# Kernel optimization log

Measured on AMD Instinct MI355X. Metric: run time of the kernel, lower is better.

## Reference

```python
import jax, jax.numpy as jnp
import numpy as np

F, H, K, T, IT, S = 128, 128, 768, 4, 2, 57  # feat, hidden, max_child, edge types, iters, num_sem


def setup_inputs() -> dict:
    key = jax.random.key(0)
    ks = jax.random.split(key, 12)

    def w(k, shape):
        fan = shape[0] if len(shape) == 2 else shape[1]
        return jax.random.normal(k, shape, jnp.float32) * fan ** -0.5

    return {
        "parent_feature": jax.random.normal(ks[0], (1, F), jnp.float32),
        "W_parent": w(ks[1], (F, H * K)), "b_parent": jnp.zeros((H * K,), jnp.float32),
        "W_exists": w(ks[2], (H, 1)), "b_exists": jnp.zeros((1,), jnp.float32),
        "W_edge_lat": w(ks[3], (2 * H, H)), "b_edge_lat": jnp.zeros((H,), jnp.float32),
        "W_edge_ex": w(ks[4], (T, H)), "b_edge_ex": jnp.zeros((T,), jnp.float32),
        "W_ne": w(ks[5], (IT, 2 * H, H)), "b_ne": jnp.zeros((IT, H), jnp.float32),
        "W_child": w(ks[6], (H * (IT + 1), H)), "b_child": jnp.zeros((H,), jnp.float32),
        "W_sem": w(ks[7], (H, S)), "b_sem": jnp.zeros((S,), jnp.float32),
        "W_child2": w(ks[8], (H, F)), "b_child2": jnp.zeros((F,), jnp.float32),
    }


def reference(parent_feature, W_parent, b_parent, W_exists, b_exists,
              W_edge_lat, b_edge_lat, W_edge_ex, b_edge_ex,
              W_ne, b_ne, W_child, b_child, W_sem, b_sem, W_child2, b_child2):
    # parent -> K child latents
    x = jax.nn.relu(parent_feature @ W_parent + b_parent)  # [1, K*H]
    cf = x.reshape(1, K, H)                                 # child feats
    exists_logits = cf @ W_exists + b_exists                # [1, K, 1]

    # pairwise edge latents [1, K, K, 2H] -> [1, K, K, H]
    pair0 = jnp.concatenate([
        jnp.broadcast_to(cf[:, :, None, :], (1, K, K, H)),
        jnp.broadcast_to(cf[:, None, :, :], (1, K, K, H))], axis=3)
    elat = jax.nn.relu(pair0 @ W_edge_lat + b_edge_lat)
    edge_logits = jnp.einsum('bijh,th->bijt', elat, W_edge_ex) + b_edge_ex  # [1,K,K,T]

    # fixed edge set: existing edges between existing nodes (dense mask form)
    exists = exists_logits[0, :, 0] > 0                     # [K]
    emask = jnp.any(edge_logits[0] > 0, axis=-1) & exists[:, None] & exists[None, :]
    any_edge = jnp.any(emask)

    feats = [cf]
    for i in range(IT):
        c = cf[0]                                           # [K, H]
        pair = jnp.concatenate([
            jnp.broadcast_to(c[:, None, :], (K, K, H)),
            jnp.broadcast_to(c[None, :, :], (K, K, H))], axis=2)
        msg = jax.nn.relu(pair @ W_ne[i] + b_ne[i])         # [K, K, H], >= 0
        msg = jnp.where(emask[:, :, None], msg, 0.0)
        # scatter_max with zeros-initialized out == max over masked neighbors (msg >= 0)
        new_cf = msg.max(axis=1)[None]                      # [1, K, H]
        cf = jnp.where(any_edge, new_cf, cf)                # no edges -> feats unchanged
        feats.append(cf)

    h = jnp.concatenate(feats, axis=2).reshape(K, H * (IT + 1))
    h = jax.nn.relu(h @ W_child + b_child)                  # [K, H]
    sem_logits = (h @ W_sem + b_sem).reshape(1, K, S)
    child_out = jax.nn.relu(h @ W_child2 + b_child2).reshape(1, K, F)
    return child_out, sem_logits, exists_logits, edge_logits
```

## Files before the change

### kernel.cpp

```cpp
#include <hip/hip_runtime.h>
#include <hip/hip_bf16.h>


#define NK 768
#define NH 128
#define NCF 98304

typedef float v2f __attribute__((ext_vector_type(2)));

__global__ __launch_bounds__(512) void k_pd(const float* __restrict__ pf,
    const float* __restrict__ Wp, const float* __restrict__ bp,
    const float* __restrict__ Wexi, const float* __restrict__ bexi,
    const float* __restrict__ Wel, const float* __restrict__ bel,
    const float* __restrict__ Wne, const float* __restrict__ Wee,
    float* __restrict__ cf0g, float* __restrict__ exO,
    float* __restrict__ A_T, float* __restrict__ BT,
    float* __restrict__ A0, float* __restrict__ B0,
    float* __restrict__ WeeT, unsigned int* __restrict__ flag)
{
    __shared__ float s_pf[128];
    __shared__ float s_cf0[2][128];
    __shared__ __align__(16) char s_scr[16384];
    int t = threadIdx.x;
    int b = blockIdx.x;
    int k0 = 2 * b;
    if (t < 128) s_pf[t] = pf[t];
    if (b == 0 && t == 0) *flag = 0u;
    if (b == 0) WeeT[(t & 127) * 4 + (t >> 7)] = Wee[t];
    __syncthreads();
    {
        float4* s_part = (float4*)s_scr;
        int c = t & 63, g = t >> 6;
        const float4* W4 = (const float4*)Wp;
        size_t base = (size_t)b * 64 + c;
        float4 acc = make_float4(0.f, 0.f, 0.f, 0.f);
        #pragma unroll
        for (int q = 0; q < 16; ++q) {
            int f = g * 16 + q;
            float4 w = W4[(size_t)f * 24576 + base];
            float p = s_pf[f];
            acc.x = fmaf(p, w.x, acc.x);
            acc.y = fmaf(p, w.y, acc.y);
            acc.z = fmaf(p, w.z, acc.z);
            acc.w = fmaf(p, w.w, acc.w);
        }
        s_part[g * 64 + c] = acc;
        __syncthreads();
        if (t < 64) {
            float4 r = s_part[t];
            #pragma unroll
            for (int g2 = 1; g2 < 8; ++g2) {
                float4 p = s_part[g2 * 64 + t];
                r.x += p.x; r.y += p.y; r.z += p.z; r.w += p.w;
            }
            float4 bi = ((const float4*)bp)[b * 64 + t];
            r.x = fmaxf(r.x + bi.x, 0.f);
            r.y = fmaxf(r.y + bi.y, 0.f);
            r.z = fmaxf(r.z + bi.z, 0.f);
            r.w = fmaxf(r.w + bi.w, 0.f);
            int row = t >> 5, h4 = t & 31;
            *(float4*)&s_cf0[row][h4 * 4] = r;
            ((float4*)cf0g)[(size_t)b * 64 + t] = r;
            float4 w = ((const float4*)Wexi)[h4];
            float dot = r.x * w.x + r.y * w.y + r.z * w.z + r.w * w.w;
            dot += __shfl_xor(dot, 16);
            dot += __shfl_xor(dot, 8);
            dot += __shfl_xor(dot, 4);
            dot += __shfl_xor(dot, 2);
            dot += __shfl_xor(dot, 1);
            if (h4 == 0) exO[k0 + row] = dot + bexi[0];
        }
    }
    __syncthreads();
    {
        float4* s_p2 = (float4*)s_scr;
        int mat = t >> 7, q = (t >> 5) & 3, c = t & 31;
        const float* W = (mat == 0) ? Wel : (mat == 1) ? (Wel + 16384)
                       : (mat == 2) ? Wne : (Wne + 16384);
        float4 a0 = make_float4(0.f, 0.f, 0.f, 0.f);
        float4 a1 = make_float4(0.f, 0.f, 0.f, 0.f);
        #pragma unroll 8
        for (int x = q * 32; x < q * 32 + 32; ++x) {
            float4 w = *(const float4*)&W[x * 128 + c * 4];
            float c0 = s_cf0[0][x], c1 = s_cf0[1][x];
            a0.x = fmaf(c0, w.x, a0.x); a0.y = fmaf(c0, w.y, a0.y);
            a0.z = fmaf(c0, w.z, a0.z); a0.w = fmaf(c0, w.w, a0.w);
            a1.x = fmaf(c1, w.x, a1.x); a1.y = fmaf(c1, w.y, a1.y);
            a1.z = fmaf(c1, w.z, a1.z); a1.w = fmaf(c1, w.w, a1.w);
        }
        s_p2[((mat * 4 + q) * 2 + 0) * 32 + c] = a0;
        s_p2[((mat * 4 + q) * 2 + 1) * 32 + c] = a1;
        __syncthreads();
        if (t < 256) {
            int m2 = t >> 6, row = (t >> 5) & 1, c2 = t & 31;
            float4 r = s_p2[((m2 * 4 + 0) * 2 + row) * 32 + c2];
            #pragma unroll
            for (int q2 = 1; q2 < 4; ++q2) {
                float4 p = s_p2[((m2 * 4 + q2) * 2 + row) * 32 + c2];
                r.x += p.x; r.y += p.y; r.z += p.z; r.w += p.w;
            }
            if (m2 == 0) {
                float4 bl = *(const float4*)&bel[c2 * 4];
                A_T[(size_t)(c2 * 4 + 0) * NK + k0 + row] = r.x + bl.x;
                A_T[(size_t)(c2 * 4 + 1) * NK + k0 + row] = r.y + bl.y;
                A_T[(size_t)(c2 * 4 + 2) * NK + k0 + row] = r.z + bl.z;
                A_T[(size_t)(c2 * 4 + 3) * NK + k0 + row] = r.w + bl.w;
            } else if (m2 == 1) {
                BT[(c2 * 4 + 0) * NK + k0 + row] = r.x;
                BT[(c2 * 4 + 1) * NK + k0 + row] = r.y;
                BT[(c2 * 4 + 2) * NK + k0 + row] = r.z;
                BT[(c2 * 4 + 3) * NK + k0 + row] = r.w;
            } else if (m2 == 2) {
                ((float4*)A0)[(size_t)(k0 + row) * 32 + c2] = r;
            } else {
                ((float4*)B0)[(size_t)(k0 + row) * 32 + c2] = r;
            }
        }
    }
}

__global__ __launch_bounds__(256) void k_edge(const float* __restrict__ A_T,
    const float* __restrict__ BT, const float* __restrict__ WeeT,
    const float* __restrict__ bex, const float* __restrict__ exO,
    float* __restrict__ edge_out, unsigned char* __restrict__ mask,
    unsigned int* __restrict__ flag)
{
    __shared__ float s_B[2][16][256];
    __shared__ float s_exi[4];
    __shared__ unsigned int s_any;
    int t = threadIdx.x;
    int i0 = blockIdx.x * 4;
    int j = blockIdx.y * 256 + t;
    float exj = exO[j];
    if (t < 4) s_exi[t] = exO[i0 + t];
    if (t == 0) s_any = 0u;
    const float4* BT4 = (const float4*)BT;
    int row = t >> 6, col = t & 63;
    {
        #pragma unroll
        for (int k = 0; k < 4; ++k)
            *(float4*)&s_B[0][row + k * 4][col * 4] =
                BT4[(size_t)(row + k * 4) * 192 + blockIdx.y * 64 + col];
    }
    __syncthreads();
    v2f l01[4] = {}, l23[4] = {};
    for (int c = 0; c < 8; ++c) {
        float4 r0, r1, r2, r3;
        if (c < 7) {
            size_t base = (size_t)((c + 1) * 16 + row) * 192 + blockIdx.y * 64 + col;
            r0 = BT4[base];
            r1 = BT4[base + 4 * 192];
            r2 = BT4[base + 8 * 192];
            r3 = BT4[base + 12 * 192];
        }
        int buf = c & 1;
        #pragma unroll
        for (int hh = 0; hh < 16; ++hh) {
            int h = c * 16 + hh;
            float4 av = *(const float4*)&A_T[(size_t)h * NK + i0];
            float4 wv = *(const float4*)&WeeT[h * 4];
            float bv = s_B[buf][hh][t];
            v2f e01 = __builtin_elementwise_max((v2f){av.x + bv, av.y + bv}, (v2f){0.f, 0.f});
            v2f e23 = __builtin_elementwise_max((v2f){av.z + bv, av.w + bv}, (v2f){0.f, 0.f});
            l01[0] += e01 * wv.x; l01[1] += e01 * wv.y;
            l01[2] += e01 * wv.z; l01[3] += e01 * wv.w;
            l23[0] += e23 * wv.x; l23[1] += e23 * wv.y;
            l23[2] += e23 * wv.z; l23[3] += e23 * wv.w;
        }
        if (c < 7) {
            int nb = (c + 1) & 1;
            *(float4*)&s_B[nb][row + 0][col * 4] = r0;
            *(float4*)&s_B[nb][row + 4][col * 4] = r1;
            *(float4*)&s_B[nb][row + 8][col * 4] = r2;
            *(float4*)&s_B[nb][row + 12][col * 4] = r3;
        }
        __syncthreads();
    }
    float b0 = bex[0], b1 = bex[1], b2 = bex[2], b3 = bex[3];
    bool ej = exj > 0.f;
    float4 v0 = make_float4(l01[0].x + b0, l01[1].x + b1, l01[2].x + b2, l01[3].x + b3);
    float4 v1 = make_float4(l01[0].y + b0, l01[1].y + b1, l01[2].y + b2, l01[3].y + b3);
    float4 v2 = make_float4(l23[0].x + b0, l23[1].x + b1, l23[2].x + b2, l23[3].x + b3);
    float4 v3 = make_float4(l23[0].y + b0, l23[1].y + b1, l23[2].y + b2, l23[3].y + b3);
    ((float4*)edge_out)[(size_t)(i0 + 0) * NK + j] = v0;
    ((float4*)edge_out)[(size_t)(i0 + 1) * NK + j] = v1;
    ((float4*)edge_out)[(size_t)(i0 + 2) * NK + j] = v2;
    ((float4*)edge_out)[(size_t)(i0 + 3) * NK + j] = v3;
    bool m0 = ((v0.x > 0.f) | (v0.y > 0.f) | (v0.z > 0.f) | (v0.w > 0.f)) && ej && (s_exi[0] > 0.f);
    bool m1 = ((v1.x > 0.f) | (v1.y > 0.f) | (v1.z > 0.f) | (v1.w > 0.f)) && ej && (s_exi[1] > 0.f);
    bool m2 = ((v2.x > 0.f) | (v2.y > 0.f) | (v2.z > 0.f) | (v2.w > 0.f)) && ej && (s_exi[2] > 0.f);
    bool m3 = ((v3.x > 0.f) | (v3.y > 0.f) | (v3.z > 0.f) | (v3.w > 0.f)) && ej && (s_exi[3] > 0.f);
    mask[(i0 + 0) * NK + j] = m0 ? (unsigned char)1 : (unsigned char)0;
    mask[(i0 + 1) * NK + j] = m1 ? (unsigned char)1 : (unsigned char)0;
    mask[(i0 + 2) * NK + j] = m2 ? (unsigned char)1 : (unsigned char)0;
    mask[(i0 + 3) * NK + j] = m3 ? (unsigned char)1 : (unsigned char)0;
    unsigned long long bal = __ballot((m0 | m1 | m2 | m3) ? 1 : 0);
    if ((t & 63) == 0 && bal) s_any = 1u;
    __syncthreads();
    if (t == 0 && s_any) *flag = 1u;
}

__global__ __launch_bounds__(256) void k_mm(const float* __restrict__ Bm,
    const unsigned char* __restrict__ mask, float* __restrict__ Mp)
{
    __shared__ float s_B[32][128];
    __shared__ float s_madd[96][8];
    int t = threadIdx.x;
    int i0 = blockIdx.x * 8;
    int j0 = blockIdx.y * 96;
    for (int idx = t; idx < 768; idx += 256) {
        int jj = idx >> 3, i = idx & 7;
        s_madd[jj][i] = mask[(i0 + i) * NK + j0 + jj] ? 0.f : -1e30f;
    }
    int p = t & 63, g = t >> 6;
    v2f M0 = {-1e30f, -1e30f}, M1 = {-1e30f, -1e30f};
    const float4* B4 = (const float4*)Bm;
    for (int c = 0; c < 3; ++c) {
        __syncthreads();
        #pragma unroll
        for (int k = 0; k < 4; ++k) {
            int idx = t + k * 256;
            ((float4*)s_B)[idx] = B4[(size_t)(j0 + c * 32) * 32 + idx];
        }
        __syncthreads();
        #pragma unroll 8
        for (int jj = 0; jj < 32; ++jj) {
            v2f b = *(const v2f*)&s_B[jj][2 * p];
            float m0 = s_madd[c * 32 + jj][2 * g];
            float m1 = s_madd[c * 32 + jj][2 * g + 1];
            M0 = __builtin_elementwise_max(M0, b + (v2f){m0, m0});
            M1 = __builtin_elementwise_max(M1, b + (v2f){m1, m1});
        }
    }
    float* Mb = Mp + (size_t)blockIdx.y * NCF;
    *(v2f*)&Mb[(i0 + 2 * g) * 128 + 2 * p] = M0;
    *(v2f*)&Mb[(i0 + 2 * g + 1) * 128 + 2 * p] = M1;
}

__global__ __launch_bounds__(512) void k_cmb1(const float* __restrict__ Mp,
    const float* __restrict__ A0, const float* __restrict__ bne,
    const float* __restrict__ cf0, const unsigned int* __restrict__ flag,
    float* __restrict__ cf1, const float* __restrict__ Wne1,
    float* __restrict__ A1, float* __restrict__ B1)
{
    __shared__ float s_cf[2][128];
    int t = threadIdx.x;
    int k0 = blockIdx.x * 2;
    unsigned int fl = *flag;
    if (t < 256) {
        int kk = t >> 7, hh = t & 127;
        int g = (k0 + kk) * 128 + hh;
        float M = Mp[g];
        #pragma unroll
        for (int q = 1; q < 8; ++q) M = fmaxf(M, Mp[q * NCF + g]);
        float v = fl ? fmaxf(A0[g] + bne[hh] + M, 0.f) : cf0[g];
        s_cf[kk][hh] = v;
        cf1[g] = v;
    }
    __syncthreads();
    int h = t & 127, kk = (t >> 7) & 1, half = t >> 8;
    const float* W = Wne1 + half * 16384;
    const float* c = &s_cf[kk][0];
    float acc = 0.f;
    #pragma unroll 8
    for (int r = 0; r < 128; ++r)
        acc = fmaf(c[r], W[r * 128 + h], acc);
    float* D = half ? B1 : A1;
    D[(k0 + kk) * 128 + h] = acc;
}

__global__ __launch_bounds__(512) void k_final(const float* __restrict__ cf0,
    const float* __restrict__ cf1, const float* __restrict__ Mp,
    const float* __restrict__ A1, const float* __restrict__ bne1,
    const unsigned int* __restrict__ flag,
    const float* __restrict__ Wc, const float* __restrict__ bc,
    const float* __restrict__ Wsem, const float* __restrict__ bsem,
    const float* __restrict__ W2, const float* __restrict__ b2,
    float* __restrict__ out)
{
    __shared__ float s_f[2][384];
    __shared__ float s_h[2][128];
    __shared__ float s_hp[2][128];
    int t = threadIdx.x;
    int k0 = blockIdx.x * 2;
    unsigned int fl = *flag;
    for (int idx = t; idx < 768; idx += 512) {
        int kk = idx >= 384 ? 1 : 0;
        int c = idx - kk * 384;
        int row = k0 + kk;
        float v;
        if (c < 128) v = cf0[row * 128 + c];
        else if (c < 256) v = cf1[row * 128 + (c - 128)];
        else {
            int hh = c - 256, g = row * 128 + hh;
            float M = Mp[g];
            #pragma unroll
            for (int q = 1; q < 8; ++q) M = fmaxf(M, Mp[q * NCF + g]);
            v = fl ? fmaxf(A1[g] + bne1[hh] + M, 0.f) : cf1[g];
        }
        s_f[kk][c] = v;
    }
    __syncthreads();
    int h = t & 127, rh = (t >> 7) & 1, kg = t >> 8;
    float acc = 0.f;
    {
        const float* f = &s_f[kg][rh * 192];
        const float* Wcp = Wc + rh * 192 * 128;
        #pragma unroll 8
        for (int r = 0; r < 192; ++r)
            acc = fmaf(f[r], Wcp[r * 128 + h], acc);
    }
    if (rh) s_hp[kg][h] = acc;
    __syncthreads();
    if (!rh) s_h[kg][h] = fmaxf(acc + s_hp[kg][h] + bc[h], 0.f);
    __syncthreads();
    float a2 = 0.f;
    {
        const float* hr = &s_h[kg][rh * 64];
        const float* W2p = W2 + rh * 64 * 128;
        #pragma unroll 8
        for (int r = 0; r < 64; ++r)
            a2 = fmaf(hr[r], W2p[r * 128 + h], a2);
    }
    if (rh) s_hp[kg][h] = a2;
    __syncthreads();
    if (!rh) out[(size_t)(k0 + kg) * 128 + h] = fmaxf(a2 + s_hp[kg][h] + b2[h], 0.f);
    if (t < 114) {
        int kk = t / 57, sidx = t - kk * 57;
        float ss = bsem[sidx];
        const float* hr = &s_h[kk][0];
        #pragma unroll 8
        for (int r = 0; r < 128; ++r)
            ss = fmaf(hr[r], Wsem[r * 57 + sidx], ss);
        out[98304 + (size_t)(k0 + kk) * 57 + sidx] = ss;
    }
}

extern "C" void kernel_launch(void* const* d_in, const int* in_sizes, int n_in,
                              void* d_out, int out_size, void* d_ws, size_t ws_size,
                              hipStream_t stream) {
    const float* pf   = (const float*)d_in[0];
    const float* Wp   = (const float*)d_in[1];
    const float* bp   = (const float*)d_in[2];
    const float* Wexi = (const float*)d_in[3];
    const float* bexi = (const float*)d_in[4];
    const float* Wel  = (const float*)d_in[5];
    const float* bel  = (const float*)d_in[6];
    const float* Wee  = (const float*)d_in[7];
    const float* bee  = (const float*)d_in[8];
    const float* Wne  = (const float*)d_in[9];
    const float* bne  = (const float*)d_in[10];
    const float* Wc   = (const float*)d_in[11];
    const float* bc   = (const float*)d_in[12];
    const float* Wsem = (const float*)d_in[13];
    const float* bsem = (const float*)d_in[14];
    const float* W2   = (const float*)d_in[15];
    const float* b2   = (const float*)d_in[16];
    float* out = (float*)d_out;
    float* ws  = (float*)d_ws;
    const int N = NCF;
    float* cf0 = ws;
    float* cf1 = ws + N;
    float* A_T = ws + 2 * N;
    float* BT  = ws + 3 * N;
    float* A0  = ws + 4 * N;
    float* B0  = ws + 5 * N;
    float* A1  = ws + 6 * N;
    float* B1  = ws + 7 * N;
    float* Mp  = ws + 8 * N;
    float* WeeT = ws + 16 * N;
    unsigned char* mask = (unsigned char*)(ws + 16 * N + 512);
    unsigned int* flag  = (unsigned int*)(mask + 589824);

    float* out_ex   = out + 142080;
    float* out_edge = out + 142848;

    k_pd<<<384, 512, 0, stream>>>(pf, Wp, bp, Wexi, bexi, Wel, bel, Wne, Wee,
                                  cf0, out_ex, A_T, BT, A0, B0, WeeT, flag);
    k_edge<<<dim3(192, 3), 256, 0, stream>>>(A_T, BT, WeeT, bee, out_ex,
                                             out_edge, mask, flag);
    k_mm<<<dim3(96, 8), 256, 0, stream>>>(B0, mask, Mp);
    k_cmb1<<<384, 512, 0, stream>>>(Mp, A0, bne, cf0, flag, cf1, Wne + 32768, A1, B1);
    k_mm<<<dim3(96, 8), 256, 0, stream>>>(B1, mask, Mp);
    k_final<<<384, 512, 0, stream>>>(cf0, cf1, Mp, A1, bne + 128, flag,
                                     Wc, bc, Wsem, bsem, W2, b2, out);
}
```

Measured before the change: 81.83 us.

## Fuse masked max-reduction into combine and final kernels, drop partial buffer

Removes the standalone masked-max kernel and its 8-way partial-max buffer. Each 2-row block of the combine and final kernels now computes the full masked max over all 768 neighbours itself: four thread groups each stream 192 rows of B from global memory, and the partial maxima are reduced in shared memory. This cuts two launches and the partial-buffer write/read round trip. In exchange, each block rereads the whole 384 KB B matrix from L2, where the old kernel reused B tiles staged in shared memory across 8 rows.

```diff
diff --git a/kernel.cpp b/kernel.cpp
--- a/kernel.cpp
+++ b/kernel.cpp
@@ -200,65 +200,48 @@
     if (t == 0 && s_any) *flag = 1u;
 }
 
-__global__ __launch_bounds__(256) void k_mm(const float* __restrict__ Bm,
-    const unsigned char* __restrict__ mask, float* __restrict__ Mp)
+__global__ __launch_bounds__(512) void k_msgA(const float* __restrict__ B0,
+    const unsigned char* __restrict__ mask, const float* __restrict__ A0,
+    const float* __restrict__ bne, const float* __restrict__ cf0,
+    const unsigned int* __restrict__ flag, float* __restrict__ cf1,
+    const float* __restrict__ Wne1, float* __restrict__ A1, float* __restrict__ B1)
 {
-    __shared__ float s_B[32][128];
-    __shared__ float s_madd[96][8];
-    int t = threadIdx.x;
-    int i0 = blockIdx.x * 8;
-    int j0 = blockIdx.y * 96;
-    for (int idx = t; idx < 768; idx += 256) {
-        int jj = idx >> 3, i = idx & 7;
-        s_madd[jj][i] = mask[(i0 + i) * NK + j0 + jj] ? 0.f : -1e30f;
-    }
-    int p = t & 63, g = t >> 6;
-    v2f M0 = {-1e30f, -1e30f}, M1 = {-1e30f, -1e30f};
-    const float4* B4 = (const float4*)Bm;
-    for (int c = 0; c < 3; ++c) {
-        __syncthreads();
-        #pragma unroll
-        for (int k = 0; k < 4; ++k) {
-            int idx = t + k * 256;
-            ((float4*)s_B)[idx] = B4[(size_t)(j0 + c * 32) * 32 + idx];
-        }
-        __syncthreads();
-        #pragma unroll 8
-        for (int jj = 0; jj < 32; ++jj) {
-            v2f b = *(const v2f*)&s_B[jj][2 * p];
-            float m0 = s_madd[c * 32 + jj][2 * g];
-            float m1 = s_madd[c * 32 + jj][2 * g + 1];
-            M0 = __builtin_elementwise_max(M0, b + (v2f){m0, m0});
-            M1 = __builtin_elementwise_max(M1, b + (v2f){m1, m1});
-        }
-    }
-    float* Mb = Mp + (size_t)blockIdx.y * NCF;
-    *(v2f*)&Mb[(i0 + 2 * g) * 128 + 2 * p] = M0;
-    *(v2f*)&Mb[(i0 + 2 * g + 1) * 128 + 2 * p] = M1;
-}
-
-__global__ __launch_bounds__(512) void k_cmb1(const float* __restrict__ Mp,
-    const float* __restrict__ A0, const float* __restrict__ bne,
-    const float* __restrict__ cf0, const unsigned int* __restrict__ flag,
-    float* __restrict__ cf1, const float* __restrict__ Wne1,
-    float* __restrict__ A1, float* __restrict__ B1)
-{
+    __shared__ float s_madd[2][768];
+    __shared__ float s_red[2][512];
     __shared__ float s_cf[2][128];
     int t = threadIdx.x;
     int k0 = blockIdx.x * 2;
+    for (int idx = t; idx < 1536; idx += 512) {
+        int r = idx >= 768 ? 1 : 0, jj = idx - r * 768;
+        s_madd[r][jj] = mask[(k0 + r) * NK + jj] ? 0.f : -1e30f;
+    }
+    __syncthreads();
+    int h = t & 127, q = t >> 7;
+    float M0 = -1e30f, M1 = -1e30f;
+    const float* bp2 = B0 + (size_t)q * 192 * 128 + h;
+    const float* ma0 = &s_madd[0][q * 192];
+    const float* ma1 = &s_madd[1][q * 192];
+    #pragma unroll 16
+    for (int jj = 0; jj < 192; ++jj) {
+        float b = bp2[jj * 128];
+        M0 = fmaxf(M0, b + ma0[jj]);
+        M1 = fmaxf(M1, b + ma1[jj]);
+    }
+    s_red[0][t] = M0;
+    s_red[1][t] = M1;
+    __syncthreads();
     unsigned int fl = *flag;
     if (t < 256) {
         int kk = t >> 7, hh = t & 127;
+        float M = fmaxf(fmaxf(s_red[kk][hh], s_red[kk][128 + hh]),
+                        fmaxf(s_red[kk][256 + hh], s_red[kk][384 + hh]));
         int g = (k0 + kk) * 128 + hh;
-        float M = Mp[g];
-        #pragma unroll
-        for (int q = 1; q < 8; ++q) M = fmaxf(M, Mp[q * NCF + g]);
         float v = fl ? fmaxf(A0[g] + bne[hh] + M, 0.f) : cf0[g];
         s_cf[kk][hh] = v;
         cf1[g] = v;
     }
     __syncthreads();
-    int h = t & 127, kk = (t >> 7) & 1, half = t >> 8;
+    int kk = (t >> 7) & 1, half = t >> 8;
     const float* W = Wne1 + half * 16384;
     const float* c = &s_cf[kk][0];
     float acc = 0.f;
@@ -269,20 +252,50 @@
     D[(k0 + kk) * 128 + h] = acc;
 }
 
-__global__ __launch_bounds__(512) void k_final(const float* __restrict__ cf0,
-    const float* __restrict__ cf1, const float* __restrict__ Mp,
-    const float* __restrict__ A1, const float* __restrict__ bne1,
-    const unsigned int* __restrict__ flag,
+__global__ __launch_bounds__(512) void k_finalf(const float* __restrict__ B1,
+    const unsigned char* __restrict__ mask, const float* __restrict__ cf0,
+    const float* __restrict__ cf1, const float* __restrict__ A1,
+    const float* __restrict__ bne1, const unsigned int* __restrict__ flag,
     const float* __restrict__ Wc, const float* __restrict__ bc,
     const float* __restrict__ Wsem, const float* __restrict__ bsem,
     const float* __restrict__ W2, const float* __restrict__ b2,
     float* __restrict__ out)
 {
+    __shared__ float s_madd[2][768];
+    __shared__ float s_red[2][512];
+    __shared__ float s_M[2][128];
     __shared__ float s_f[2][384];
     __shared__ float s_h[2][128];
     __shared__ float s_hp[2][128];
     int t = threadIdx.x;
     int k0 = blockIdx.x * 2;
+    for (int idx = t; idx < 1536; idx += 512) {
+        int r = idx >= 768 ? 1 : 0, jj = idx - r * 768;
+        s_madd[r][jj] = mask[(k0 + r) * NK + jj] ? 0.f : -1e30f;
+    }
+    __syncthreads();
+    int h = t & 127, q = t >> 7;
+    {
+        float M0 = -1e30f, M1 = -1e30f;
+        const float* bp2 = B1 + (size_t)q * 192 * 128 + h;
+        const float* ma0 = &s_madd[0][q * 192];
+        const float* ma1 = &s_madd[1][q * 192];
+        #pragma unroll 16
+        for (int jj = 0; jj < 192; ++jj) {
+            float b = bp2[jj * 128];
+            M0 = fmaxf(M0, b + ma0[jj]);
+            M1 = fmaxf(M1, b + ma1[jj]);
+        }
+        s_red[0][t] = M0;
+        s_red[1][t] = M1;
+    }
+    __syncthreads();
+    if (t < 256) {
+        int kk = t >> 7, hh = t & 127;
+        s_M[kk][hh] = fmaxf(fmaxf(s_red[kk][hh], s_red[kk][128 + hh]),
+                            fmaxf(s_red[kk][256 + hh], s_red[kk][384 + hh]));
+    }
+    __syncthreads();
     unsigned int fl = *flag;
     for (int idx = t; idx < 768; idx += 512) {
         int kk = idx >= 384 ? 1 : 0;
@@ -293,15 +306,12 @@
         else if (c < 256) v = cf1[row * 128 + (c - 128)];
         else {
             int hh = c - 256, g = row * 128 + hh;
-            float M = Mp[g];
-            #pragma unroll
-            for (int q = 1; q < 8; ++q) M = fmaxf(M, Mp[q * NCF + g]);
-            v = fl ? fmaxf(A1[g] + bne1[hh] + M, 0.f) : cf1[g];
+            v = fl ? fmaxf(A1[g] + bne1[hh] + s_M[kk][hh], 0.f) : cf1[g];
         }
         s_f[kk][c] = v;
     }
     __syncthreads();
-    int h = t & 127, rh = (t >> 7) & 1, kg = t >> 8;
+    int rh = (t >> 7) & 1, kg = t >> 8;
     float acc = 0.f;
     {
         const float* f = &s_f[kg][rh * 192];
@@ -367,9 +377,8 @@
     float* B0  = ws + 5 * N;
     float* A1  = ws + 6 * N;
     float* B1  = ws + 7 * N;
-    float* Mp  = ws + 8 * N;
-    float* WeeT = ws + 16 * N;
-    unsigned char* mask = (unsigned char*)(ws + 16 * N + 512);
+    float* WeeT = ws + 8 * N;
+    unsigned char* mask = (unsigned char*)(ws + 8 * N + 512);
     unsigned int* flag  = (unsigned int*)(mask + 589824);
 
     float* out_ex   = out + 142080;
@@ -379,9 +388,8 @@
                                   cf0, out_ex, A_T, BT, A0, B0, WeeT, flag);
     k_edge<<<dim3(192, 3), 256, 0, stream>>>(A_T, BT, WeeT, bee, out_ex,
                                              out_edge, mask, flag);
-    k_mm<<<dim3(96, 8), 256, 0, stream>>>(B0, mask, Mp);
-    k_cmb1<<<384, 512, 0, stream>>>(Mp, A0, bne, cf0, flag, cf1, Wne + 32768, A1, B1);
-    k_mm<<<dim3(96, 8), 256, 0, stream>>>(B1, mask, Mp);
-    k_final<<<384, 512, 0, stream>>>(cf0, cf1, Mp, A1, bne + 128, flag,
-                                     Wc, bc, Wsem, bsem, W2, b2, out);
-}
+    k_msgA<<<384, 512, 0, stream>>>(B0, mask, A0, bne, cf0, flag, cf1,
+                                    Wne + 32768, A1, B1);
+    k_finalf<<<384, 512, 0, stream>>>(B1, mask, cf0, cf1, A1, bne + 128, flag,
+                                      Wc, bc, Wsem, bsem, W2, b2, out);
+}
```

New measurement: 76.16 us. 6.9% less time.
